# Kernel tuning notes

Measured on AMD Instinct MI355X. Metric: run time of the kernel, lower is better.

The kernel has to match this reference:

```python
import jax, jax.numpy as jnp
import numpy as np

B, S, I, C, P = 64, 14, 32, 10, 4   # batch, spatial, in-caps/pos, classes, pose size
ROUTINGS = 3
EPS = 1e-9


def setup_inputs() -> dict:
    key = jax.random.key(0)
    k1, k2, k3, k4, k5 = jax.random.split(key, 5)
    return {
        "inputs_pose": jax.random.normal(k1, (B, S, S, I, P, P), jnp.float32),
        "inputs_activation": jax.random.uniform(k2, (B, S, S, I), jnp.float32),
        "w": jax.random.normal(k3, (1, I, C, P, P), jnp.float32),
        "beta_v": jax.random.normal(k4, (1, C), jnp.float32) * 0.1,
        "beta_a": jax.random.normal(k5, (1, C), jnp.float32) * 0.1,
    }


def _em_routing(votes, i_act, beta_v, beta_a, routings):
    # votes: [B, N, C, 16], i_act: [B, N]
    Bn, N, Cc, D = votes.shape
    rr = jnp.full((Bn, N, Cc, 1), 1.0 / Cc, votes.dtype)  # uniform init assignments
    bv = beta_v.reshape(1, 1, Cc, 1)
    ba = beta_a.reshape(1, 1, Cc, 1)
    it_min, it_max = 1.0, min(float(routings), 3.0)  # inverse-temperature schedule
    o_mean = o_act = None
    for it in range(routings):
        inv_temp = it_min + (it_max - it_min) * it / max(1.0, routings - 1.0)
        # --- M step ---
        rr_p = rr * i_act[:, :, None, None]                        # [B,N,C,1]
        rr_sum = jnp.sum(rr_p, axis=1, keepdims=True)              # [B,1,C,1]
        o_mean = jnp.sum(rr_p * votes, axis=1, keepdims=True) / rr_sum   # [B,1,C,16]
        o_var = jnp.sum(rr_p * jnp.square(votes - o_mean), axis=1, keepdims=True) / rr_sum
        o_stdv = jnp.sqrt(o_var)                                   # [B,1,C,16]
        cost = jnp.sum((bv + jnp.log(o_stdv + EPS)) * rr_sum, axis=-1, keepdims=True)  # [B,1,C,1]
        o_act = jax.nn.sigmoid(inv_temp * (ba - cost))             # [B,1,C,1]
        # --- E step (skipped on last iteration) ---
        if it < routings - 1:
            logp = (-jnp.sum(jnp.square(votes - o_mean) / (2.0 * jnp.square(o_stdv) + EPS),
                             axis=-1, keepdims=True)
                    - jnp.sum(jnp.log(o_stdv + EPS), axis=-1, keepdims=True))  # [B,N,C,1]
            zz = jnp.log(o_act + EPS) + logp
            rr = jax.nn.softmax(zz, axis=2)
    return o_mean[:, 0], o_act[:, 0, :, 0]  # [B,C,16], [B,C]


def reference(inputs_pose, inputs_activation, w, beta_v, beta_a):
    # mat_transform: votes[b,h,w,i,c] = pose[b,h,w,i] @ W[i,c]   (4x4 matmuls)
    votes = jnp.einsum('bhwipq,icqr->bhwicpr', inputs_pose, w[0])
    votes = votes.reshape(B, S, S, I, C, P * P)
    # coordinate addition: scaled (row+0.5)/S onto pose element 0, col onto element 1
    coord = (jnp.arange(S, dtype=votes.dtype) + 0.5) / S
    votes = votes.at[..., 0].add(coord[None, :, None, None, None])
    votes = votes.at[..., 1].add(coord[None, None, :, None, None])
    votes = votes.reshape(B, S * S * I, C, P * P)
    acts = inputs_activation.reshape(B, S * S * I)
    o_mean, o_act = _em_routing(votes, acts, beta_v, beta_a, ROUTINGS)
    pose = o_mean.reshape(B, C, P, P)
    return pose, o_act
```

## Files before the change

### kernel.cpp

```cpp
#include <hip/hip_runtime.h>
#include <math.h>

#define Bsz 64
#define Ssz 14
#define Isz 32
#define Csz 10
#define Dsz 16
#define Nsz (Ssz*Ssz*Isz)
#define EPSF 1e-9f

#define CH   640
#define NCH  10
#define MCH  1568
#define MROW 72
#define PRMS 36
#define BC   (Bsz*Csz)

template<int CTRL, int RMASK>
__device__ __forceinline__ float dpp_add(float x) {
    int y = __builtin_amdgcn_update_dpp(0, __float_as_int(x), CTRL, RMASK, 0xf, true);
    return x + __int_as_float(y);
}
__device__ __forceinline__ float wave_sum64(float x) {
    x = dpp_add<0x111, 0xf>(x);
    x = dpp_add<0x112, 0xf>(x);
    x = dpp_add<0x114, 0xf>(x);
    x = dpp_add<0x118, 0xf>(x);
    x = dpp_add<0x142, 0xa>(x);
    x = dpp_add<0x143, 0xc>(x);
    return x;
}

__global__ __launch_bounds__(640) void mom_kernel(
    const float* __restrict__ pose,
    const float* __restrict__ act,
    float* __restrict__ partM)
{
    const int b = blockIdx.x, mch = blockIdx.y;
    const int tid = threadIdx.x, lane = tid & 63;

    __shared__ float Macc[32][73];

    float s[69];
#pragma unroll
    for (int j = 0; j < 69; ++j) s[j] = 0.f;

    const float* poseb = pose + (size_t)b*Nsz*Dsz;
    const float* actb  = act  + (size_t)b*Nsz;
    const int base = mch*MCH;

    for (int k = 0; k < MCH; k += 640) {
        const int nl = k + tid;
        if (nl < MCH) {
            const int n = base + nl;
            const float4* pp = reinterpret_cast<const float4*>(poseb + (size_t)n*Dsz);
            float4 a0 = pp[0], a1 = pp[1], a2 = pp[2], a3 = pp[3];
            float p[16] = {a0.x,a0.y,a0.z,a0.w, a1.x,a1.y,a1.z,a1.w,
                           a2.x,a2.y,a2.z,a2.w, a3.x,a3.y,a3.z,a3.w};
            const int hw = n >> 5, wc = hw % Ssz, hr = hw / Ssz;
            const float chh = (hr+0.5f)*(1.f/Ssz), cww = (wc+0.5f)*(1.f/Ssz);
            const float wgt = actb[n]*(1.f/Csz);
            s[0] += wgt;
            float wp[16];
#pragma unroll
            for (int j = 0; j < 16; ++j) { wp[j] = wgt*p[j]; s[1+j] += wp[j]; }
            int t = 17;
#pragma unroll
            for (int pr = 0; pr < 4; ++pr)
#pragma unroll
                for (int k1 = 0; k1 < 4; ++k1)
#pragma unroll
                    for (int k2 = k1; k2 < 4; ++k2)
                        s[t++] += wp[pr*4+k1]*p[pr*4+k2];
            const float wch = wgt*chh, wcw = wgt*cww;
#pragma unroll
            for (int j = 0; j < 4; ++j) { s[57+j] += wch*p[j]; s[61+j] += wcw*p[j]; }
            s[65] += wch; s[66] += wcw; s[67] += wch*chh; s[68] += wcw*cww;
        }
    }
#pragma unroll
    for (int j = 0; j < 69; ++j) s[j] += __shfl_xor(s[j], 32);

    for (int t = tid; t < 32*73; t += 640) (&Macc[0][0])[t] = 0.f;
    __syncthreads();
    if (lane < 32) {
#pragma unroll
        for (int j = 0; j < 69; ++j) atomicAdd(&Macc[lane][j], s[j]);
    }
    __syncthreads();
    for (int t = tid; t < 32*MROW; t += 640) {
        const int i = t / MROW, j = t - i*MROW;
        if (j < 69) atomicAdd(&partM[(size_t)b*(32*MROW) + t], Macc[i][j]);
    }
}

template<bool FIRST>
__global__ __launch_bounds__(640) void em_kernel(
    const float* __restrict__ pose, const float* __restrict__ act,
    const float* __restrict__ w, const float* __restrict__ beta_v,
    const float* __restrict__ beta_a, const float* __restrict__ partIn,
    float* __restrict__ partOut, float inv_temp_prev)
{
    const int b = blockIdx.x, chunk = blockIdx.y;
    const int tid = threadIdx.x, wv_ = tid >> 6, lane = tid & 63;

    __shared__ float Wm[Csz][Isz*17];
    __shared__ float U2[Csz*CH];
    __shared__ float prm[Csz][PRMS];
    __shared__ float pl[Csz*Dsz];
    __shared__ float s0sh;

    for (int t = tid; t < Csz*Isz*Dsz; t += 640) {
        const int cc = t >> 9, rem = t & 511, i = rem >> 4, q = rem & 15;
        Wm[cc][i*17 + q] = w[(i*Csz + cc)*Dsz + q];
    }
    if (FIRST) {
        for (int t = tid; t < 32*MROW; t += 640) {
            const int i = t / MROW, j = t - i*MROW;
            U2[i*73 + j] = partIn[(size_t)b*(32*MROW) + t];
        }
    } else {
        if (tid < Csz*33) {
            const int c2 = tid / 33, j = tid - c2*33;
            float sacc = 0.f;
            const float* pb = partIn + (size_t)j*BC + b*Csz + c2;
            for (int ch = 0; ch < NCH; ++ch) sacc += pb[(size_t)ch*33*BC];
            U2[c2*34 + j] = sacc;
        }
    }
    __syncthreads();

    if (tid < Csz*Dsz) {
        const int c = tid >> 4, d = tid & 15;
        if (FIRST) {
            const int pr = d >> 2, r = d & 3;
            float S0 = 0.f, S1 = 0.f, S2 = 0.f;
            for (int i = 0; i < 32; ++i) {
                const float* Mi = U2 + i*73;
                const float* Wi = &Wm[c][i*17];
                S0 += Mi[0];
                const float w0 = Wi[r], w1 = Wi[4+r], w2 = Wi[8+r], w3 = Wi[12+r];
                const float* M1 = Mi + 1 + pr*4;
                S1 += w0*M1[0] + w1*M1[1] + w2*M1[2] + w3*M1[3];
                const float* Q = Mi + 17 + pr*10;
                S2 += w0*w0*Q[0] + w1*w1*Q[4] + w2*w2*Q[7] + w3*w3*Q[9]
                    + 2.f*(w0*w1*Q[1] + w0*w2*Q[2] + w0*w3*Q[3]
                         + w1*w2*Q[5] + w1*w3*Q[6] + w2*w3*Q[8]);
                if (d == 0) {
                    S1 += Mi[65];
                    S2 += 2.f*(w0*Mi[57] + w1*Mi[58] + w2*Mi[59] + w3*Mi[60]) + Mi[67];
                } else if (d == 1) {
                    S1 += Mi[66];
                    S2 += 2.f*(w0*Mi[61] + w1*Mi[62] + w2*Mi[63] + w3*Mi[64]) + Mi[68];
                }
            }
            const float mean = S1 / S0;
            const float var = fmaxf(S2/S0 - mean*mean, 0.f);
            prm[c][d]    = mean;
            prm[c][16+d] = 1.f/(2.f*var + EPSF);
            pl[tid]      = __logf(sqrtf(var) + EPSF);
            if (tid == 0) s0sh = S0;
        } else {
            const float S0 = U2[c*34];
            const float mn = U2[c*34 + 1 + d] / S0;
            const float var = fmaxf(U2[c*34 + 17 + d]/S0 - mn*mn, 0.f);
            prm[c][d]    = mn;
            prm[c][16+d] = 1.f/(2.f*var + EPSF);
            pl[tid]      = __logf(sqrtf(var) + EPSF);
        }
    }
    __syncthreads();
    if (tid < Csz) {
        float sumlog = 0.f;
#pragma unroll
        for (int d = 0; d < 16; ++d) sumlog += pl[tid*16 + d];
        const float S0 = FIRST ? s0sh : U2[tid*34];
        const float cost = S0*(16.f*beta_v[tid] + sumlog);
        const float oact = 1.f/(1.f + __expf(-inv_temp_prev*(beta_a[tid] - cost)));
        prm[tid][32] = __logf(oact + EPSF) - sumlog;
    }
    __syncthreads();

    const int base = chunk*CH;
    const float* poseb = pose + (size_t)b*Nsz*Dsz;

    {
        const int c = wv_;
        float W16[16];
#pragma unroll
        for (int j = 0; j < 16; ++j) W16[j] = Wm[c][(lane & 31)*17 + j];
        const float pv = (lane < 33) ? prm[c][lane] : 0.f;
        const int pvi = __float_as_int(pv);
        float m_s[16], g_s[16];
#pragma unroll
        for (int d = 0; d < 16; ++d) {
            m_s[d] = __int_as_float(__builtin_amdgcn_readlane(pvi, d));
            g_s[d] = __int_as_float(__builtin_amdgcn_readlane(pvi, 16 + d));
        }
        const float K_s = __int_as_float(__builtin_amdgcn_readlane(pvi, 32));

        for (int k = 0; k < CH; k += 64) {
            const int n = base + k + lane;
            if (n < Nsz) {
                const float4* pp = reinterpret_cast<const float4*>(poseb + (size_t)n*Dsz);
                float4 a0 = pp[0], a1 = pp[1], a2 = pp[2], a3 = pp[3];
                float p[16] = {a0.x,a0.y,a0.z,a0.w, a1.x,a1.y,a1.z,a1.w,
                               a2.x,a2.y,a2.z,a2.w, a3.x,a3.y,a3.z,a3.w};
                const int hw = n >> 5, wc2 = hw % Ssz, hr2 = hw / Ssz;
                const float chh = (hr2+0.5f)*(1.f/Ssz), cww = (wc2+0.5f)*(1.f/Ssz);
                float quad = 0.f;
#pragma unroll
                for (int pr = 0; pr < 4; ++pr) {
#pragma unroll
                    for (int r = 0; r < 4; ++r) {
                        float vvv = p[pr*4]*W16[r] + p[pr*4+1]*W16[4+r]
                                  + p[pr*4+2]*W16[8+r] + p[pr*4+3]*W16[12+r];
                        if (pr == 0 && r == 0) vvv += chh;
                        if (pr == 0 && r == 1) vvv += cww;
                        const float dv = vvv - m_s[pr*4+r];
                        quad += dv*dv*g_s[pr*4+r];
                    }
                }
                U2[c*CH + k + lane] = K_s - quad;
            }
        }
    }
    __syncthreads();

    {
        const int n = base + tid;
        if (n < Nsz) {
            float z[Csz];
#pragma unroll
            for (int cc = 0; cc < Csz; ++cc) z[cc] = U2[cc*CH + tid];
            float zmax = z[0];
#pragma unroll
            for (int cc = 1; cc < Csz; ++cc) zmax = fmaxf(zmax, z[cc]);
            float zsum = 0.f;
#pragma unroll
            for (int cc = 0; cc < Csz; ++cc) { z[cc] = __expf(z[cc] - zmax); zsum += z[cc]; }
            const float sc = __fdividef(act[(size_t)b*Nsz + n], zsum);
#pragma unroll
            for (int cc = 0; cc < Csz; ++cc) U2[cc*CH + tid] = z[cc]*sc;
        }
    }
    __syncthreads();

    {
        const int c = wv_;
        float W16[16];
#pragma unroll
        for (int j = 0; j < 16; ++j) W16[j] = Wm[c][(lane & 31)*17 + j];
        float s0 = 0.f, s1[16], s2[16];
#pragma unroll
        for (int d = 0; d < 16; ++d) { s1[d] = 0.f; s2[d] = 0.f; }
        for (int k = 0; k < CH; k += 64) {
            const int nl = k + lane, n = base + nl;
            if (n < Nsz) {
                const float4* pp = reinterpret_cast<const float4*>(poseb + (size_t)n*Dsz);
                const int hw = n >> 5, wc2 = hw % Ssz, hr2 = hw / Ssz;
                const float chh = (hr2+0.5f)*(1.f/Ssz), cww = (wc2+0.5f)*(1.f/Ssz);
                const float wgt = U2[c*CH + nl];
                s0 += wgt;
#pragma unroll
                for (int pr = 0; pr < 4; ++pr) {
                    const float4 pv4 = pp[pr];
#pragma unroll
                    for (int r = 0; r < 4; ++r) {
                        float vv = pv4.x*W16[r] + pv4.y*W16[4+r] + pv4.z*W16[8+r] + pv4.w*W16[12+r];
                        if (pr == 0 && r == 0) vv += chh;
                        if (pr == 0 && r == 1) vv += cww;
                        const float wvv = wgt*vv;
                        s1[pr*4+r] += wvv;
                        s2[pr*4+r] += wvv*vv;
                    }
                }
            }
        }
        s0 = wave_sum64(s0);
#pragma unroll
        for (int d = 0; d < 16; ++d) { s1[d] = wave_sum64(s1[d]); s2[d] = wave_sum64(s2[d]); }
        if (lane == 63) {
            float* pt = partOut + (size_t)chunk*33*BC + b*Csz + c;
            pt[0] = s0;
#pragma unroll
            for (int d = 0; d < 16; ++d) {
                pt[(size_t)(1+d)*BC]  = s1[d];
                pt[(size_t)(17+d)*BC] = s2[d];
            }
        }
    }
}

__global__ __launch_bounds__(64) void fin_kernel(
    const float* __restrict__ partC, const float* __restrict__ beta_v,
    const float* __restrict__ beta_a, float* __restrict__ out, float inv_temp)
{
    const int bc = blockIdx.x*64 + threadIdx.x;
    const int c = bc % Csz;
    float S[33];
#pragma unroll
    for (int j = 0; j < 33; ++j) S[j] = 0.f;
    for (int ch = 0; ch < NCH; ++ch) {
        const float* pb = partC + (size_t)ch*33*BC + bc;
#pragma unroll
        for (int j = 0; j < 33; ++j) S[j] += pb[(size_t)j*BC];
    }
    const float S0 = S[0], rS0 = 1.f/S0;
    float sumlog = 0.f;
#pragma unroll
    for (int d = 0; d < 16; ++d) {
        const float mn = S[1+d]*rS0;
        const float var = fmaxf(S[17+d]*rS0 - mn*mn, 0.f);
        out[(size_t)bc*Dsz + d] = mn;
        sumlog += __logf(sqrtf(var) + EPSF);
    }
    const float cost = S0*(16.f*beta_v[c] + sumlog);
    out[(size_t)Bsz*Csz*Dsz + bc] = 1.f/(1.f + __expf(-inv_temp*(beta_a[c] - cost)));
}

extern "C" void kernel_launch(void* const* d_in, const int* in_sizes, int n_in,
                              void* d_out, int out_size, void* d_ws, size_t ws_size,
                              hipStream_t stream)
{
    (void)in_sizes; (void)n_in; (void)out_size; (void)ws_size;
    const float* pose = (const float*)d_in[0];
    const float* act  = (const float*)d_in[1];
    const float* w    = (const float*)d_in[2];
    const float* bv   = (const float*)d_in[3];
    const float* ba   = (const float*)d_in[4];
    float* out = (float*)d_out;

    float* regA = (float*)d_ws;
    float* regB = regA + (size_t)NCH*33*BC;
    float* partM  = regA;
    float* partC  = regB;
    float* partC2 = regA;

    hipMemsetAsync(partM, 0, (size_t)Bsz*32*MROW*sizeof(float), stream);
    mom_kernel      <<<dim3(Bsz, 4),   640, 0, stream>>>(pose, act, partM);
    em_kernel<true> <<<dim3(Bsz, NCH), 640, 0, stream>>>(pose, act, w, bv, ba, partM, partC, 1.0f);
    em_kernel<false><<<dim3(Bsz, NCH), 640, 0, stream>>>(pose, act, w, bv, ba, partC, partC2, 2.0f);
    fin_kernel      <<<NCH,             64, 0, stream>>>(partC2, bv, ba, out, 3.0f);
}
```

Baseline: 256.4 us.

## Fuse moment, EM iterations, and finalize into single per-batch persistent kernel

Replaces the memset, moment kernel, two EM kernels and finalize kernel with one kernel that uses a single block per batch element. The block computes the moments, then runs both E/M iterations over all chunks internally, keeping the sufficient statistics in shared memory. This removes launch overhead, global partial-sum traffic and cross-kernel reductions. In exchange the grid shrinks from hundreds of blocks to 64, so each block processes every chunk serially and most CUs sit idle.

```diff
diff --git a/kernel.cpp b/kernel.cpp
--- a/kernel.cpp
+++ b/kernel.cpp
@@ -11,10 +11,6 @@
 
 #define CH   640
 #define NCH  10
-#define MCH  1568
-#define MROW 72
-#define PRMS 36
-#define BC   (Bsz*Csz)
 
 template<int CTRL, int RMASK>
 __device__ __forceinline__ float dpp_add(float x) {
@@ -31,299 +27,265 @@
     return x;
 }
 
-__global__ __launch_bounds__(640) void mom_kernel(
+__global__ __launch_bounds__(640) void cap_kernel(
     const float* __restrict__ pose,
     const float* __restrict__ act,
-    float* __restrict__ partM)
+    const float* __restrict__ w,
+    const float* __restrict__ beta_v,
+    const float* __restrict__ beta_a,
+    float* __restrict__ out)
 {
-    const int b = blockIdx.x, mch = blockIdx.y;
-    const int tid = threadIdx.x, lane = tid & 63;
-
-    __shared__ float Macc[32][73];
-
-    float s[69];
-#pragma unroll
-    for (int j = 0; j < 69; ++j) s[j] = 0.f;
-
-    const float* poseb = pose + (size_t)b*Nsz*Dsz;
-    const float* actb  = act  + (size_t)b*Nsz;
-    const int base = mch*MCH;
-
-    for (int k = 0; k < MCH; k += 640) {
-        const int nl = k + tid;
-        if (nl < MCH) {
-            const int n = base + nl;
-            const float4* pp = reinterpret_cast<const float4*>(poseb + (size_t)n*Dsz);
-            float4 a0 = pp[0], a1 = pp[1], a2 = pp[2], a3 = pp[3];
-            float p[16] = {a0.x,a0.y,a0.z,a0.w, a1.x,a1.y,a1.z,a1.w,
-                           a2.x,a2.y,a2.z,a2.w, a3.x,a3.y,a3.z,a3.w};
-            const int hw = n >> 5, wc = hw % Ssz, hr = hw / Ssz;
-            const float chh = (hr+0.5f)*(1.f/Ssz), cww = (wc+0.5f)*(1.f/Ssz);
-            const float wgt = actb[n]*(1.f/Csz);
-            s[0] += wgt;
-            float wp[16];
-#pragma unroll
-            for (int j = 0; j < 16; ++j) { wp[j] = wgt*p[j]; s[1+j] += wp[j]; }
-            int t = 17;
-#pragma unroll
-            for (int pr = 0; pr < 4; ++pr)
-#pragma unroll
-                for (int k1 = 0; k1 < 4; ++k1)
-#pragma unroll
-                    for (int k2 = k1; k2 < 4; ++k2)
-                        s[t++] += wp[pr*4+k1]*p[pr*4+k2];
-            const float wch = wgt*chh, wcw = wgt*cww;
-#pragma unroll
-            for (int j = 0; j < 4; ++j) { s[57+j] += wch*p[j]; s[61+j] += wcw*p[j]; }
-            s[65] += wch; s[66] += wcw; s[67] += wch*chh; s[68] += wcw*cww;
-        }
-    }
-#pragma unroll
-    for (int j = 0; j < 69; ++j) s[j] += __shfl_xor(s[j], 32);
-
-    for (int t = tid; t < 32*73; t += 640) (&Macc[0][0])[t] = 0.f;
-    __syncthreads();
-    if (lane < 32) {
-#pragma unroll
-        for (int j = 0; j < 69; ++j) atomicAdd(&Macc[lane][j], s[j]);
-    }
-    __syncthreads();
-    for (int t = tid; t < 32*MROW; t += 640) {
-        const int i = t / MROW, j = t - i*MROW;
-        if (j < 69) atomicAdd(&partM[(size_t)b*(32*MROW) + t], Macc[i][j]);
-    }
-}
-
-template<bool FIRST>
-__global__ __launch_bounds__(640) void em_kernel(
-    const float* __restrict__ pose, const float* __restrict__ act,
-    const float* __restrict__ w, const float* __restrict__ beta_v,
-    const float* __restrict__ beta_a, const float* __restrict__ partIn,
-    float* __restrict__ partOut, float inv_temp_prev)
-{
-    const int b = blockIdx.x, chunk = blockIdx.y;
+    const int b = blockIdx.x;
     const int tid = threadIdx.x, wv_ = tid >> 6, lane = tid & 63;
 
     __shared__ float Wm[Csz][Isz*17];
     __shared__ float U2[Csz*CH];
-    __shared__ float prm[Csz][PRMS];
+    __shared__ float Macc[32][73];
+    __shared__ float prm[Csz][36];
     __shared__ float pl[Csz*Dsz];
-    __shared__ float s0sh;
+    __shared__ float Sv[Csz][34];
 
     for (int t = tid; t < Csz*Isz*Dsz; t += 640) {
         const int cc = t >> 9, rem = t & 511, i = rem >> 4, q = rem & 15;
         Wm[cc][i*17 + q] = w[(i*Csz + cc)*Dsz + q];
     }
-    if (FIRST) {
-        for (int t = tid; t < 32*MROW; t += 640) {
-            const int i = t / MROW, j = t - i*MROW;
-            U2[i*73 + j] = partIn[(size_t)b*(32*MROW) + t];
-        }
-    } else {
-        if (tid < Csz*33) {
-            const int c2 = tid / 33, j = tid - c2*33;
-            float sacc = 0.f;
-            const float* pb = partIn + (size_t)j*BC + b*Csz + c2;
-            for (int ch = 0; ch < NCH; ++ch) sacc += pb[(size_t)ch*33*BC];
-            U2[c2*34 + j] = sacc;
-        }
-    }
+    for (int t = tid; t < 32*73; t += 640) (&Macc[0][0])[t] = 0.f;
     __syncthreads();
 
-    if (tid < Csz*Dsz) {
-        const int c = tid >> 4, d = tid & 15;
-        if (FIRST) {
-            const int pr = d >> 2, r = d & 3;
-            float S0 = 0.f, S1 = 0.f, S2 = 0.f;
-            for (int i = 0; i < 32; ++i) {
-                const float* Mi = U2 + i*73;
-                const float* Wi = &Wm[c][i*17];
-                S0 += Mi[0];
-                const float w0 = Wi[r], w1 = Wi[4+r], w2 = Wi[8+r], w3 = Wi[12+r];
-                const float* M1 = Mi + 1 + pr*4;
-                S1 += w0*M1[0] + w1*M1[1] + w2*M1[2] + w3*M1[3];
-                const float* Q = Mi + 17 + pr*10;
-                S2 += w0*w0*Q[0] + w1*w1*Q[4] + w2*w2*Q[7] + w3*w3*Q[9]
-                    + 2.f*(w0*w1*Q[1] + w0*w2*Q[2] + w0*w3*Q[3]
-                         + w1*w2*Q[5] + w1*w3*Q[6] + w2*w3*Q[8]);
-                if (d == 0) {
-                    S1 += Mi[65];
-                    S2 += 2.f*(w0*Mi[57] + w1*Mi[58] + w2*Mi[59] + w3*Mi[60]) + Mi[67];
-                } else if (d == 1) {
-                    S1 += Mi[66];
-                    S2 += 2.f*(w0*Mi[61] + w1*Mi[62] + w2*Mi[63] + w3*Mi[64]) + Mi[68];
-                }
-            }
-            const float mean = S1 / S0;
-            const float var = fmaxf(S2/S0 - mean*mean, 0.f);
-            prm[c][d]    = mean;
-            prm[c][16+d] = 1.f/(2.f*var + EPSF);
-            pl[tid]      = __logf(sqrtf(var) + EPSF);
-            if (tid == 0) s0sh = S0;
-        } else {
-            const float S0 = U2[c*34];
-            const float mn = U2[c*34 + 1 + d] / S0;
-            const float var = fmaxf(U2[c*34 + 17 + d]/S0 - mn*mn, 0.f);
-            prm[c][d]    = mn;
-            prm[c][16+d] = 1.f/(2.f*var + EPSF);
-            pl[tid]      = __logf(sqrtf(var) + EPSF);
-        }
-    }
-    __syncthreads();
-    if (tid < Csz) {
-        float sumlog = 0.f;
-#pragma unroll
-        for (int d = 0; d < 16; ++d) sumlog += pl[tid*16 + d];
-        const float S0 = FIRST ? s0sh : U2[tid*34];
-        const float cost = S0*(16.f*beta_v[tid] + sumlog);
-        const float oact = 1.f/(1.f + __expf(-inv_temp_prev*(beta_a[tid] - cost)));
-        prm[tid][32] = __logf(oact + EPSF) - sumlog;
-    }
-    __syncthreads();
-
-    const int base = chunk*CH;
     const float* poseb = pose + (size_t)b*Nsz*Dsz;
+    const float* actb  = act  + (size_t)b*Nsz;
 
     {
-        const int c = wv_;
-        float W16[16];
-#pragma unroll
-        for (int j = 0; j < 16; ++j) W16[j] = Wm[c][(lane & 31)*17 + j];
-        const float pv = (lane < 33) ? prm[c][lane] : 0.f;
-        const int pvi = __float_as_int(pv);
-        float m_s[16], g_s[16];
-#pragma unroll
-        for (int d = 0; d < 16; ++d) {
-            m_s[d] = __int_as_float(__builtin_amdgcn_readlane(pvi, d));
-            g_s[d] = __int_as_float(__builtin_amdgcn_readlane(pvi, 16 + d));
-        }
-        const float K_s = __int_as_float(__builtin_amdgcn_readlane(pvi, 32));
-
-        for (int k = 0; k < CH; k += 64) {
-            const int n = base + k + lane;
+        float s[69];
+#pragma unroll
+        for (int j = 0; j < 69; ++j) s[j] = 0.f;
+        for (int k = 0; k < Nsz; k += CH) {
+            const int n = k + tid;
             if (n < Nsz) {
                 const float4* pp = reinterpret_cast<const float4*>(poseb + (size_t)n*Dsz);
                 float4 a0 = pp[0], a1 = pp[1], a2 = pp[2], a3 = pp[3];
                 float p[16] = {a0.x,a0.y,a0.z,a0.w, a1.x,a1.y,a1.z,a1.w,
                                a2.x,a2.y,a2.z,a2.w, a3.x,a3.y,a3.z,a3.w};
-                const int hw = n >> 5, wc2 = hw % Ssz, hr2 = hw / Ssz;
-                const float chh = (hr2+0.5f)*(1.f/Ssz), cww = (wc2+0.5f)*(1.f/Ssz);
-                float quad = 0.f;
-#pragma unroll
-                for (int pr = 0; pr < 4; ++pr) {
-#pragma unroll
-                    for (int r = 0; r < 4; ++r) {
-                        float vvv = p[pr*4]*W16[r] + p[pr*4+1]*W16[4+r]
-                                  + p[pr*4+2]*W16[8+r] + p[pr*4+3]*W16[12+r];
-                        if (pr == 0 && r == 0) vvv += chh;
-                        if (pr == 0 && r == 1) vvv += cww;
-                        const float dv = vvv - m_s[pr*4+r];
-                        quad += dv*dv*g_s[pr*4+r];
+                const int hw = n >> 5, wc = hw % Ssz, hr = hw / Ssz;
+                const float chh = (hr+0.5f)*(1.f/Ssz), cww = (wc+0.5f)*(1.f/Ssz);
+                const float wgt = actb[n]*(1.f/Csz);
+                s[0] += wgt;
+                float wp[16];
+#pragma unroll
+                for (int j = 0; j < 16; ++j) { wp[j] = wgt*p[j]; s[1+j] += wp[j]; }
+                int t = 17;
+#pragma unroll
+                for (int pr = 0; pr < 4; ++pr)
+#pragma unroll
+                    for (int k1 = 0; k1 < 4; ++k1)
+#pragma unroll
+                        for (int k2 = k1; k2 < 4; ++k2)
+                            s[t++] += wp[pr*4+k1]*p[pr*4+k2];
+                const float wch = wgt*chh, wcw = wgt*cww;
+#pragma unroll
+                for (int j = 0; j < 4; ++j) { s[57+j] += wch*p[j]; s[61+j] += wcw*p[j]; }
+                s[65] += wch; s[66] += wcw; s[67] += wch*chh; s[68] += wcw*cww;
+            }
+        }
+#pragma unroll
+        for (int j = 0; j < 69; ++j) s[j] += __shfl_xor(s[j], 32);
+        if (lane < 32) {
+#pragma unroll
+            for (int j = 0; j < 69; ++j) atomicAdd(&Macc[lane][j], s[j]);
+        }
+    }
+    __syncthreads();
+
+    {
+        const int c = tid >> 6, d = (tid >> 2) & 15, g = tid & 3;
+        const int pr = d >> 2, r = d & 3;
+        float S0 = 0.f, S1 = 0.f, S2 = 0.f;
+#pragma unroll
+        for (int ii = 0; ii < 8; ++ii) {
+            const int i = g*8 + ii;
+            const float* Mi = Macc[i];
+            const float* Wi = &Wm[c][i*17];
+            S0 += Mi[0];
+            const float w0 = Wi[r], w1 = Wi[4+r], w2 = Wi[8+r], w3 = Wi[12+r];
+            const float* M1 = Mi + 1 + pr*4;
+            S1 += w0*M1[0] + w1*M1[1] + w2*M1[2] + w3*M1[3];
+            const float* Q = Mi + 17 + pr*10;
+            S2 += w0*w0*Q[0] + w1*w1*Q[4] + w2*w2*Q[7] + w3*w3*Q[9]
+                + 2.f*(w0*w1*Q[1] + w0*w2*Q[2] + w0*w3*Q[3]
+                     + w1*w2*Q[5] + w1*w3*Q[6] + w2*w3*Q[8]);
+            if (d == 0) {
+                S1 += Mi[65];
+                S2 += 2.f*(w0*Mi[57] + w1*Mi[58] + w2*Mi[59] + w3*Mi[60]) + Mi[67];
+            } else if (d == 1) {
+                S1 += Mi[66];
+                S2 += 2.f*(w0*Mi[61] + w1*Mi[62] + w2*Mi[63] + w3*Mi[64]) + Mi[68];
+            }
+        }
+        U2[tid] = S0; U2[640 + tid] = S1; U2[1280 + tid] = S2;
+        __syncthreads();
+        if (g == 0) {
+            float T0 = 0.f, T1 = 0.f, T2 = 0.f;
+#pragma unroll
+            for (int kk = 0; kk < 4; ++kk) {
+                T0 += U2[tid + kk]; T1 += U2[640 + tid + kk]; T2 += U2[1280 + tid + kk];
+            }
+            const float mean = T1 / T0;
+            const float var = fmaxf(T2/T0 - mean*mean, 0.f);
+            prm[c][d]    = mean;
+            prm[c][16+d] = 1.f/(2.f*var + EPSF);
+            pl[tid >> 2] = __logf(sqrtf(var) + EPSF);
+            if (d == 0) Sv[c][0] = T0;
+        }
+        __syncthreads();
+        if (tid < Csz) {
+            float sumlog = 0.f;
+#pragma unroll
+            for (int d2 = 0; d2 < 16; ++d2) sumlog += pl[tid*16 + d2];
+            const float cost = Sv[tid][0]*(16.f*beta_v[tid] + sumlog);
+            const float oact = 1.f/(1.f + __expf(-1.0f*(beta_a[tid] - cost)));
+            prm[tid][32] = __logf(oact + EPSF) - sumlog;
+        }
+        __syncthreads();
+    }
+
+    for (int iter = 0; iter < 2; ++iter) {
+        const int c = wv_;
+        float W16[16];
+#pragma unroll
+        for (int j = 0; j < 16; ++j) W16[j] = Wm[c][(lane & 31)*17 + j];
+        const float pv = (lane < 33) ? prm[c][lane] : 0.f;
+        const int pvi = __float_as_int(pv);
+        float m_s[16], g_s[16];
+#pragma unroll
+        for (int d = 0; d < 16; ++d) {
+            m_s[d] = __int_as_float(__builtin_amdgcn_readlane(pvi, d));
+            g_s[d] = __int_as_float(__builtin_amdgcn_readlane(pvi, 16 + d));
+        }
+        const float K_s = __int_as_float(__builtin_amdgcn_readlane(pvi, 32));
+
+        float s0 = 0.f, s1[16], s2[16];
+#pragma unroll
+        for (int d = 0; d < 16; ++d) { s1[d] = 0.f; s2[d] = 0.f; }
+
+        for (int chunk = 0; chunk < NCH; ++chunk) {
+            const int base = chunk*CH;
+
+            for (int k = 0; k < CH; k += 64) {
+                const int n = base + k + lane;
+                if (n < Nsz) {
+                    const float4* pp = reinterpret_cast<const float4*>(poseb + (size_t)n*Dsz);
+                    float4 a0 = pp[0], a1 = pp[1], a2 = pp[2], a3 = pp[3];
+                    float p[16] = {a0.x,a0.y,a0.z,a0.w, a1.x,a1.y,a1.z,a1.w,
+                                   a2.x,a2.y,a2.z,a2.w, a3.x,a3.y,a3.z,a3.w};
+                    const int hw = n >> 5, wc2 = hw % Ssz, hr2 = hw / Ssz;
+                    const float chh = (hr2+0.5f)*(1.f/Ssz), cww = (wc2+0.5f)*(1.f/Ssz);
+                    float quad = 0.f;
+#pragma unroll
+                    for (int pr = 0; pr < 4; ++pr) {
+#pragma unroll
+                        for (int r = 0; r < 4; ++r) {
+                            float vvv = p[pr*4]*W16[r] + p[pr*4+1]*W16[4+r]
+                                      + p[pr*4+2]*W16[8+r] + p[pr*4+3]*W16[12+r];
+                            if (pr == 0 && r == 0) vvv += chh;
+                            if (pr == 0 && r == 1) vvv += cww;
+                            const float dv = vvv - m_s[pr*4+r];
+                            quad += dv*dv*g_s[pr*4+r];
+                        }
+                    }
+                    U2[c*CH + k + lane] = K_s - quad;
+                }
+            }
+            __syncthreads();
+
+            {
+                const int n = base + tid;
+                if (n < Nsz) {
+                    float z[Csz];
+#pragma unroll
+                    for (int cc = 0; cc < Csz; ++cc) z[cc] = U2[cc*CH + tid];
+                    float zmax = z[0];
+#pragma unroll
+                    for (int cc = 1; cc < Csz; ++cc) zmax = fmaxf(zmax, z[cc]);
+                    float zsum = 0.f;
+#pragma unroll
+                    for (int cc = 0; cc < Csz; ++cc) { z[cc] = __expf(z[cc] - zmax); zsum += z[cc]; }
+                    const float sc = __fdividef(actb[n], zsum);
+#pragma unroll
+                    for (int cc = 0; cc < Csz; ++cc) U2[cc*CH + tid] = z[cc]*sc;
+                }
+            }
+            __syncthreads();
+
+            for (int k = 0; k < CH; k += 64) {
+                const int n = base + k + lane;
+                if (n < Nsz) {
+                    const float4* pp = reinterpret_cast<const float4*>(poseb + (size_t)n*Dsz);
+                    const int hw = n >> 5, wc2 = hw % Ssz, hr2 = hw / Ssz;
+                    const float chh = (hr2+0.5f)*(1.f/Ssz), cww = (wc2+0.5f)*(1.f/Ssz);
+                    const float wgt = U2[c*CH + k + lane];
+                    s0 += wgt;
+#pragma unroll
+                    for (int pr = 0; pr < 4; ++pr) {
+                        const float4 pv4 = pp[pr];
+#pragma unroll
+                        for (int r = 0; r < 4; ++r) {
+                            float vv = pv4.x*W16[r] + pv4.y*W16[4+r]
+                                     + pv4.z*W16[8+r] + pv4.w*W16[12+r];
+                            if (pr == 0 && r == 0) vv += chh;
+                            if (pr == 0 && r == 1) vv += cww;
+                            const float wvv = wgt*vv;
+                            s1[pr*4+r] += wvv;
+                            s2[pr*4+r] += wvv*vv;
+                        }
                     }
                 }
-                U2[c*CH + k + lane] = K_s - quad;
-            }
-        }
-    }
-    __syncthreads();
-
-    {
-        const int n = base + tid;
-        if (n < Nsz) {
-            float z[Csz];
-#pragma unroll
-            for (int cc = 0; cc < Csz; ++cc) z[cc] = U2[cc*CH + tid];
-            float zmax = z[0];
-#pragma unroll
-            for (int cc = 1; cc < Csz; ++cc) zmax = fmaxf(zmax, z[cc]);
-            float zsum = 0.f;
-#pragma unroll
-            for (int cc = 0; cc < Csz; ++cc) { z[cc] = __expf(z[cc] - zmax); zsum += z[cc]; }
-            const float sc = __fdividef(act[(size_t)b*Nsz + n], zsum);
-#pragma unroll
-            for (int cc = 0; cc < Csz; ++cc) U2[cc*CH + tid] = z[cc]*sc;
-        }
-    }
-    __syncthreads();
-
-    {
-        const int c = wv_;
-        float W16[16];
-#pragma unroll
-        for (int j = 0; j < 16; ++j) W16[j] = Wm[c][(lane & 31)*17 + j];
-        float s0 = 0.f, s1[16], s2[16];
-#pragma unroll
-        for (int d = 0; d < 16; ++d) { s1[d] = 0.f; s2[d] = 0.f; }
-        for (int k = 0; k < CH; k += 64) {
-            const int nl = k + lane, n = base + nl;
-            if (n < Nsz) {
-                const float4* pp = reinterpret_cast<const float4*>(poseb + (size_t)n*Dsz);
-                const int hw = n >> 5, wc2 = hw % Ssz, hr2 = hw / Ssz;
-                const float chh = (hr2+0.5f)*(1.f/Ssz), cww = (wc2+0.5f)*(1.f/Ssz);
-                const float wgt = U2[c*CH + nl];
-                s0 += wgt;
-#pragma unroll
-                for (int pr = 0; pr < 4; ++pr) {
-                    const float4 pv4 = pp[pr];
-#pragma unroll
-                    for (int r = 0; r < 4; ++r) {
-                        float vv = pv4.x*W16[r] + pv4.y*W16[4+r] + pv4.z*W16[8+r] + pv4.w*W16[12+r];
-                        if (pr == 0 && r == 0) vv += chh;
-                        if (pr == 0 && r == 1) vv += cww;
-                        const float wvv = wgt*vv;
-                        s1[pr*4+r] += wvv;
-                        s2[pr*4+r] += wvv*vv;
-                    }
-                }
-            }
-        }
+            }
+        }
+
         s0 = wave_sum64(s0);
 #pragma unroll
         for (int d = 0; d < 16; ++d) { s1[d] = wave_sum64(s1[d]); s2[d] = wave_sum64(s2[d]); }
         if (lane == 63) {
-            float* pt = partOut + (size_t)chunk*33*BC + b*Csz + c;
-            pt[0] = s0;
-#pragma unroll
-            for (int d = 0; d < 16; ++d) {
-                pt[(size_t)(1+d)*BC]  = s1[d];
-                pt[(size_t)(17+d)*BC] = s2[d];
-            }
-        }
-    }
-}
-
-__global__ __launch_bounds__(64) void fin_kernel(
-    const float* __restrict__ partC, const float* __restrict__ beta_v,
-    const float* __restrict__ beta_a, float* __restrict__ out, float inv_temp)
-{
-    const int bc = blockIdx.x*64 + threadIdx.x;
-    const int c = bc % Csz;
-    float S[33];
-#pragma unroll
-    for (int j = 0; j < 33; ++j) S[j] = 0.f;
-    for (int ch = 0; ch < NCH; ++ch) {
-        const float* pb = partC + (size_t)ch*33*BC + bc;
-#pragma unroll
-        for (int j = 0; j < 33; ++j) S[j] += pb[(size_t)j*BC];
-    }
-    const float S0 = S[0], rS0 = 1.f/S0;
-    float sumlog = 0.f;
-#pragma unroll
-    for (int d = 0; d < 16; ++d) {
-        const float mn = S[1+d]*rS0;
-        const float var = fmaxf(S[17+d]*rS0 - mn*mn, 0.f);
-        out[(size_t)bc*Dsz + d] = mn;
-        sumlog += __logf(sqrtf(var) + EPSF);
-    }
-    const float cost = S0*(16.f*beta_v[c] + sumlog);
-    out[(size_t)Bsz*Csz*Dsz + bc] = 1.f/(1.f + __expf(-inv_temp*(beta_a[c] - cost)));
+            Sv[c][0] = s0;
+#pragma unroll
+            for (int d = 0; d < 16; ++d) { Sv[c][1+d] = s1[d]; Sv[c][17+d] = s2[d]; }
+        }
+        __syncthreads();
+
+        const float invt = (iter == 0) ? 2.0f : 3.0f;
+        if (tid < Csz*Dsz) {
+            const int c2 = tid >> 4, d = tid & 15;
+            const float T0 = Sv[c2][0];
+            const float mn = Sv[c2][1+d] / T0;
+            const float var = fmaxf(Sv[c2][17+d]/T0 - mn*mn, 0.f);
+            if (iter == 1) {
+                out[((size_t)b*Csz + c2)*Dsz + d] = mn;
+            } else {
+                prm[c2][d]    = mn;
+                prm[c2][16+d] = 1.f/(2.f*var + EPSF);
+            }
+            pl[tid] = __logf(sqrtf(var) + EPSF);
+        }
+        __syncthreads();
+        if (tid < Csz) {
+            float sumlog = 0.f;
+#pragma unroll
+            for (int d2 = 0; d2 < 16; ++d2) sumlog += pl[tid*16 + d2];
+            const float T0 = Sv[tid][0];
+            const float cost = T0*(16.f*beta_v[tid] + sumlog);
+            const float oact = 1.f/(1.f + __expf(-invt*(beta_a[tid] - cost)));
+            if (iter == 1) out[(size_t)Bsz*Csz*Dsz + b*Csz + tid] = oact;
+            else           prm[tid][32] = __logf(oact + EPSF) - sumlog;
+        }
+        __syncthreads();
+    }
 }
 
 extern "C" void kernel_launch(void* const* d_in, const int* in_sizes, int n_in,
                               void* d_out, int out_size, void* d_ws, size_t ws_size,
                               hipStream_t stream)
 {
-    (void)in_sizes; (void)n_in; (void)out_size; (void)ws_size;
+    (void)in_sizes; (void)n_in; (void)out_size; (void)d_ws; (void)ws_size;
     const float* pose = (const float*)d_in[0];
     const float* act  = (const float*)d_in[1];
     const float* w    = (const float*)d_in[2];
@@ -331,15 +293,5 @@
     const float* ba   = (const float*)d_in[4];
     float* out = (float*)d_out;
 
-    float* regA = (float*)d_ws;
-    float* regB = regA + (size_t)NCH*33*BC;
-    float* partM  = regA;
-    float* partC  = regB;
-    float* partC2 = regA;
-
-    hipMemsetAsync(partM, 0, (size_t)Bsz*32*MROW*sizeof(float), stream);
-    mom_kernel      <<<dim3(Bsz, 4),   640, 0, stream>>>(pose, act, partM);
-    em_kernel<true> <<<dim3(Bsz, NCH), 640, 0, stream>>>(pose, act, w, bv, ba, partM, partC, 1.0f);
-    em_kernel<false><<<dim3(Bsz, NCH), 640, 0, stream>>>(pose, act, w, bv, ba, partC, partC2, 2.0f);
-    fin_kernel      <<<NCH,             64, 0, stream>>>(partC2, bv, ba, out, 3.0f);
-}
+    cap_kernel<<<Bsz, CH, 0, stream>>>(pose, act, w, bv, ba, out);
+}
```

Measured after the change: 426.0 us. 1.66x slower.
